# Optimization experiments

Measured on AMD Instinct MI355X. Metric: run time of the kernel, lower is better.

Reference implementation:

```python
import jax, jax.numpy as jnp
import numpy as np

N_NODES = 50000
D = 128
E_RAND = 640000
ALPHA = 0.2  # LeakyReLU negative slope


def setup_inputs() -> dict:
    key = jax.random.key(0)
    k1, k2, k3, k4, k5 = jax.random.split(key, 5)
    inputs = jax.random.normal(k1, (N_NODES, D), dtype=jnp.float32) * 0.1
    # xavier_normal with gain=1.414 as in the torch module
    W = jax.random.normal(k2, (D, D), dtype=jnp.float32) * (1.414 * np.sqrt(2.0 / (D + D)))
    a = jax.random.normal(k3, (2 * D,), dtype=jnp.float32) * (1.414 * np.sqrt(2.0 / (1 + 2 * D)))
    # random edges + self-loops so every node has at least one outgoing edge (nonzero rowsum)
    src = jnp.concatenate([jax.random.randint(k4, (E_RAND,), 0, N_NODES), jnp.arange(N_NODES)])
    dst = jnp.concatenate([jax.random.randint(k5, (E_RAND,), 0, N_NODES), jnp.arange(N_NODES)])
    edge = jnp.stack([src, dst]).astype(jnp.int64)
    return {"inputs": inputs, "edge": edge, "W": W, "a": a}


def reference(inputs, edge, W, a):
    N = inputs.shape[0]
    src, dst = edge[0], edge[1]
    h = inputs @ W  # [N, D]
    # a @ [h_src; h_dst] per edge == h_src @ a[:D] + h_dst @ a[D:]
    score = h[src] @ a[:D] + h[dst] @ a[D:]  # [E]
    edge_e = jnp.exp(jax.nn.leaky_relu(score, negative_slope=ALPHA))  # [E]
    # sparse.mm(coo(edge, edge_e), ones): rowsum over src (coalesce sums duplicates)
    e_rowsum = jax.ops.segment_sum(edge_e, src, num_segments=N)  # [N]
    # sparse.mm(coo(edge, edge_e), h): weighted aggregation of h[dst] into src rows
    h_prime = jax.ops.segment_sum(edge_e[:, None] * h[dst], src, num_segments=N)  # [N, D]
    h_prime = h_prime / e_rowsum[:, None]
    return jax.nn.elu(h_prime)
```

## Files before the change

kernel.cpp:

```cpp
#include <hip/hip_runtime.h>
#include <hip/hip_bf16.h>


constexpr int D    = 128;
constexpr int CH   = 8192;
constexpr int NPB  = 128;
constexpr int CAPB = 2048;

typedef __attribute__((ext_vector_type(8))) short bf16x8;
typedef __attribute__((ext_vector_type(4))) float f32x4;

__device__ __forceinline__ short f2bf(float f) {
    unsigned u = __float_as_uint(f);
    unsigned r = (u + 0x7fffu + ((u >> 16) & 1u)) >> 16;
    return (short)r;
}
__device__ __forceinline__ float bf2f(short b) {
    return __uint_as_float(((unsigned)(unsigned short)b) << 16);
}
__device__ __forceinline__ short2 pk_bf16(float x, float y) {
    __hip_bfloat162 bb = __float22bfloat162_rn(make_float2(x, y));
    short2 r;
    __builtin_memcpy(&r, &bb, 4);
    return r;
}

__global__ __launch_bounds__(256) void init(const float* __restrict__ W,
                                            short* __restrict__ bw,
                                            int* __restrict__ bcnt, int NB) {
    if (blockIdx.x == 8) {
        for (int u = threadIdx.x; u < NB; u += 256) bcnt[u] = 0;
        return;
    }
    const int tid = blockIdx.x * 256 + threadIdx.x;
    const int l = tid & 63, st = tid >> 6;
    const int s = st >> 3, t = st & 7;
    const int n = t * 16 + (l & 15);
    const int q = l >> 4;
#pragma unroll
    for (int j = 0; j < 8; ++j) {
        const int k = s * 32 + q * 8 + j;
        bw[tid * 8 + j] = f2bf(W[k * D + n]);
    }
}

__global__ __launch_bounds__(256) void bin_and_gemm(
    const float* __restrict__ X, const short* __restrict__ bw,
    const float* __restrict__ a,
    const int* __restrict__ src, const int* __restrict__ dst,
    int* __restrict__ bcnt, int* __restrict__ binned,
    short* __restrict__ h, float* __restrict__ s1, float* __restrict__ s2,
    int NB, int NC, int N, int E) {
    __shared__ int hist[392], hbase[392];
    __shared__ short lbw[16384];
    if (blockIdx.x < (unsigned)NC) {
        const int c = blockIdx.x, t = threadIdx.x;
        for (int u = t; u < NB; u += 256) hist[u] = 0;
        __syncthreads();
        const int lo = c * CH, hi = min(lo + CH, E);
        const int hi4 = lo + ((hi - lo) & ~3);
        for (int i = lo + t * 4; i < hi4; i += 1024) {
            const int4 s4 = *(const int4*)(src + i);
            atomicAdd(&hist[s4.x >> 7], 1);
            atomicAdd(&hist[s4.y >> 7], 1);
            atomicAdd(&hist[s4.z >> 7], 1);
            atomicAdd(&hist[s4.w >> 7], 1);
        }
        for (int i = hi4 + t; i < hi; i += 256)
            atomicAdd(&hist[src[i] >> 7], 1);
        __syncthreads();
        for (int u = t; u < NB; u += 256) {
            hbase[u] = atomicAdd(&bcnt[u], hist[u]);
            hist[u] = 0;
        }
        __syncthreads();
        for (int i = lo + t * 4; i < hi4; i += 1024) {
            const int4 s4 = *(const int4*)(src + i);
            const int4 d4 = *(const int4*)(dst + i);
            const int sv[4] = {s4.x, s4.y, s4.z, s4.w};
            const int dv[4] = {d4.x, d4.y, d4.z, d4.w};
#pragma unroll
            for (int j = 0; j < 4; ++j) {
                const int b = sv[j] >> 7;
                const int r = atomicAdd(&hist[b], 1);
                const int idx = hbase[b] + r;
                if (idx < CAPB)
                    binned[b * CAPB + idx] = ((sv[j] & 127) << 16) | dv[j];
            }
        }
        for (int i = hi4 + t; i < hi; i += 256) {
            const int s = src[i];
            const int b = s >> 7;
            const int r = atomicAdd(&hist[b], 1);
            const int idx = hbase[b] + r;
            if (idx < CAPB)
                binned[b * CAPB + idx] = ((s & 127) << 16) | dst[i];
        }
        return;
    }
    {
        int4* lb4 = (int4*)lbw;
        const int4* gb4 = (const int4*)bw;
#pragma unroll
        for (int it = 0; it < 8; ++it)
            lb4[it * 256 + threadIdx.x] = gb4[it * 256 + threadIdx.x];
    }
    __syncthreads();
    const int wave = threadIdx.x >> 6, lane = threadIdx.x & 63;
    const int r0 = (blockIdx.x - NC) * 64 + wave * 16;
    const int m = lane & 15, q = lane >> 4;
    const int arow = r0 + m;
    const bool rowok = arow < N;
    const float* xp = X + (size_t)arow * D + q * 8;

    f32x4 acc[8] = {};
#pragma unroll
    for (int s = 0; s < 4; ++s) {
        float4 xa = {0, 0, 0, 0}, xb = {0, 0, 0, 0};
        if (rowok) {
            xa = *(const float4*)(xp + s * 32);
            xb = *(const float4*)(xp + s * 32 + 4);
        }
        bf16x8 af;
        short2 c0 = pk_bf16(xa.x, xa.y), c1 = pk_bf16(xa.z, xa.w);
        short2 c2 = pk_bf16(xb.x, xb.y), c3 = pk_bf16(xb.z, xb.w);
        af[0] = c0.x; af[1] = c0.y; af[2] = c1.x; af[3] = c1.y;
        af[4] = c2.x; af[5] = c2.y; af[6] = c3.x; af[7] = c3.y;
#pragma unroll
        for (int t = 0; t < 8; ++t) {
            bf16x8 bf = *(const bf16x8*)(lbw + ((s * 8 + t) * 64 + lane) * 8);
            acc[t] = __builtin_amdgcn_mfma_f32_16x16x32_bf16(af, bf, acc[t], 0, 0, 0);
        }
    }
    float a1v[8], a2v[8];
#pragma unroll
    for (int t = 0; t < 8; ++t) {
        a1v[t] = a[t * 16 + m];
        a2v[t] = a[D + t * 16 + m];
    }
    float p1[4] = {0, 0, 0, 0}, p2[4] = {0, 0, 0, 0};
#pragma unroll
    for (int t = 0; t < 8; ++t) {
        short2 h01 = pk_bf16(acc[t][0], acc[t][1]);
        short2 h23 = pk_bf16(acc[t][2], acc[t][3]);
        const short hb[4] = {h01.x, h01.y, h23.x, h23.y};
#pragma unroll
        for (int i = 0; i < 4; ++i) {
            const int row = r0 + q * 4 + i;
            if (row < N) h[(size_t)row * D + t * 16 + m] = hb[i];
            const float hr = bf2f(hb[i]);
            p1[i] += hr * a1v[t];
            p2[i] += hr * a2v[t];
        }
    }
#pragma unroll
    for (int off = 1; off < 16; off <<= 1) {
#pragma unroll
        for (int i = 0; i < 4; ++i) {
            p1[i] += __shfl_xor(p1[i], off);
            p2[i] += __shfl_xor(p2[i], off);
        }
    }
    if (m < 4) {
        const int row = r0 + q * 4 + m;
        if (row < N) {
            const float v1 = (m == 0) ? p1[0] : (m == 1) ? p1[1] : (m == 2) ? p1[2] : p1[3];
            const float v2 = (m == 0) ? p2[0] : (m == 1) ? p2[1] : (m == 2) ? p2[2] : p2[3];
            s1[row] = v1;
            s2[row] = v2;
        }
    }
}

__global__ __launch_bounds__(1024) void aggregate(
    const int* __restrict__ binned, const int* __restrict__ bcnt,
    const float* __restrict__ s1, const float* __restrict__ s2,
    const short* __restrict__ h, float* __restrict__ out, int N) {
    __shared__ int elist[CAPB];
    __shared__ unsigned short dlist[CAPB];
    __shared__ int ncnt[NPB], snc[NPB], exclp[NPB], pcnt[NPB];
    __shared__ float ss1[NPB];
    const int b = blockIdx.x, tid = threadIdx.x;
    const int nb0 = b * NPB;
    if (tid < NPB) {
        ncnt[tid] = 0;
        pcnt[tid] = 0;
        ss1[tid] = (nb0 + tid < N) ? s1[nb0 + tid] : 0.f;
    }
    __syncthreads();
    const int nE = min(bcnt[b], CAPB);
    for (int i = tid; i < nE; i += 1024) {
        const int e = binned[b * CAPB + i];
        elist[i] = e;
        atomicAdd(&ncnt[e >> 16], 1);
    }
    __syncthreads();
    if (tid < NPB) snc[tid] = ncnt[tid];
    __syncthreads();
    for (int o = 1; o < NPB; o <<= 1) {
        const int v = (tid < NPB && tid >= o) ? snc[tid - o] : 0;
        __syncthreads();
        if (tid < NPB) snc[tid] += v;
        __syncthreads();
    }
    if (tid < NPB) exclp[tid] = snc[tid] - ncnt[tid];
    __syncthreads();
    for (int i = tid; i < nE; i += 1024) {
        const int e = elist[i];
        const int r = e >> 16;
        const int k = atomicAdd(&pcnt[r], 1);
        dlist[exclp[r] + k] = (unsigned short)(e & 0xFFFF);
    }
    __syncthreads();

    const int wid = tid >> 6, lane = tid & 63;
    const int g = lane >> 4, m = lane & 15;
#pragma unroll 1
    for (int t = 0; t < 8; ++t) {
        const int r = wid * 8 + t;
        const int n = nb0 + r;
        if (n >= N) continue;
        const int cnt = ncnt[r];
        if (cnt == 0) continue;
        const int beg = exclp[r];
        const float s1n = ss1[r];

        int dA0 = dlist[beg + min(g, cnt - 1)];
        int dB0 = dlist[beg + min(4 + g, cnt - 1)];
        float  sA0 = s2[dA0], sB0 = s2[dB0];
        bf16x8 rA0 = *(const bf16x8*)(h + (size_t)dA0 * D + m * 8);
        bf16x8 rB0 = *(const bf16x8*)(h + (size_t)dB0 * D + m * 8);

        float acc[8] = {};
        float rs = 0.f;
        for (int k0 = 0; k0 < cnt; k0 += 8) {
            const bool more = (k0 + 8) < cnt;
            float sA1, sB1;
            bf16x8 rA1, rB1;
            int dA1, dB1;
            if (more) {
                dA1 = dlist[beg + min(k0 + 8 + g, cnt - 1)];
                dB1 = dlist[beg + min(k0 + 12 + g, cnt - 1)];
                sA1 = s2[dA1];
                sB1 = s2[dB1];
                rA1 = *(const bf16x8*)(h + (size_t)dA1 * D + m * 8);
                rB1 = *(const bf16x8*)(h + (size_t)dB1 * D + m * 8);
            }
            float scA = s1n + sA0;
            scA = scA > 0.f ? scA : 0.2f * scA;
            float eA = __expf(scA);
            if (k0 + g >= cnt) eA = 0.f;
            float scB = s1n + sB0;
            scB = scB > 0.f ? scB : 0.2f * scB;
            float eB = __expf(scB);
            if (k0 + 4 + g >= cnt) eB = 0.f;
#pragma unroll
            for (int j = 0; j < 8; ++j)
                acc[j] += eA * bf2f(rA0[j]) + eB * bf2f(rB0[j]);
            rs += eA + eB;
            if (more) { sA0 = sA1; sB0 = sB1; rA0 = rA1; rB0 = rB1; }
        }
#pragma unroll
        for (int off = 16; off <= 32; off <<= 1) {
            rs += __shfl_xor(rs, off);
#pragma unroll
            for (int j = 0; j < 8; ++j) acc[j] += __shfl_xor(acc[j], off);
        }
        if (g == 0) {
            const float inv = 1.f / rs;
            float o[8];
#pragma unroll
            for (int j = 0; j < 8; ++j) {
                float v = acc[j] * inv;
                o[j] = v > 0.f ? v : expm1f(v);
            }
            float* op = out + (size_t)n * D + m * 8;
            *(float4*)op       = make_float4(o[0], o[1], o[2], o[3]);
            *(float4*)(op + 4) = make_float4(o[4], o[5], o[6], o[7]);
        }
    }
}

extern "C" void kernel_launch(void* const* d_in, const int* in_sizes, int n_in,
                              void* d_out, int out_size, void* d_ws, size_t ws_size,
                              hipStream_t stream) {
    const float* X    = (const float*)d_in[0];
    const int*   edge = (const int*)d_in[1];
    const float* W    = (const float*)d_in[2];
    const float* a    = (const float*)d_in[3];
    float* out = (float*)d_out;

    const int N = in_sizes[0] / D;
    const int E = in_sizes[1] / 2;
    const int* src = edge;
    const int* dst = edge + E;

    const int NB = (N + NPB - 1) / NPB;
    const int NC = (E + CH - 1) / CH;
    const int NG = (N + 63) / 64;

    char* ws = (char*)d_ws;
    short* h    = (short*)ws; ws += (size_t)N * D * sizeof(short);
    int* binned = (int*)ws;   ws += (size_t)NB * CAPB * sizeof(int);
    short* bw   = (short*)ws; ws += 2048 * 8 * sizeof(short);
    float* s1   = (float*)ws; ws += (size_t)N * sizeof(float);
    float* s2   = (float*)ws; ws += (size_t)N * sizeof(float);
    int* bcnt   = (int*)ws;   ws += (size_t)NB * sizeof(int);

    init<<<9, 256, 0, stream>>>(W, bw, bcnt, NB);
    bin_and_gemm<<<NC + NG, 256, 0, stream>>>(X, bw, a, src, dst, bcnt, binned,
                                              h, s1, s2, NB, NC, N, E);
    aggregate<<<NB, 1024, 0, stream>>>(binned, bcnt, s1, s2, h, out, N);
}
```

Before: 145.8 us.

## Split aggregate bins across two 512-thread blocks with wave-shuffle scan

Each 128-node bin is now handled by two 512-thread blocks, each taking 64 nodes and filtering the bin's edges by half. The block-wide LDS prefix scan with many barriers is replaced by a single-wave shuffle scan. The dlist is padded with zeros so the per-edge clamps go away. 32-bit index math and __expf-based ELU replace the size_t math and expm1f. The trade-off is that every edge in a bin is loaded and scanned twice, and ELU loses some precision for small negatives.

Result: faster. 133.9 us (-8.1%).

```diff
diff --git a/kernel.cpp b/kernel.cpp
--- a/kernel.cpp
+++ b/kernel.cpp
@@ -6,6 +6,7 @@
 constexpr int CH   = 8192;
 constexpr int NPB  = 128;
 constexpr int CAPB = 2048;
+constexpr int DCAP = 2064;
 
 typedef __attribute__((ext_vector_type(8))) short bf16x8;
 typedef __attribute__((ext_vector_type(4))) float f32x4;
@@ -172,64 +173,73 @@
     }
 }
 
-__global__ __launch_bounds__(1024) void aggregate(
+__global__ __launch_bounds__(512) void aggregate(
     const int* __restrict__ binned, const int* __restrict__ bcnt,
     const float* __restrict__ s1, const float* __restrict__ s2,
     const short* __restrict__ h, float* __restrict__ out, int N) {
     __shared__ int elist[CAPB];
-    __shared__ unsigned short dlist[CAPB];
-    __shared__ int ncnt[NPB], snc[NPB], exclp[NPB], pcnt[NPB];
-    __shared__ float ss1[NPB];
-    const int b = blockIdx.x, tid = threadIdx.x;
-    const int nb0 = b * NPB;
-    if (tid < NPB) {
+    __shared__ unsigned short dlist[DCAP];
+    __shared__ int ncnt[64], exclp[64], pcnt[64];
+    __shared__ float ss1[64];
+    const int blk = blockIdx.x, tid = threadIdx.x;
+    const int b = blk >> 1, half = blk & 1;
+    const int n0 = b * NPB + half * 64;
+    if (tid < 64) {
         ncnt[tid] = 0;
         pcnt[tid] = 0;
-        ss1[tid] = (nb0 + tid < N) ? s1[nb0 + tid] : 0.f;
+        ss1[tid] = (n0 + tid < N) ? s1[n0 + tid] : 0.f;
     }
     __syncthreads();
     const int nE = min(bcnt[b], CAPB);
-    for (int i = tid; i < nE; i += 1024) {
+    const int hbit = half << 6;
+    for (int i = tid; i < nE; i += 512) {
         const int e = binned[b * CAPB + i];
         elist[i] = e;
-        atomicAdd(&ncnt[e >> 16], 1);
-    }
-    __syncthreads();
-    if (tid < NPB) snc[tid] = ncnt[tid];
-    __syncthreads();
-    for (int o = 1; o < NPB; o <<= 1) {
-        const int v = (tid < NPB && tid >= o) ? snc[tid - o] : 0;
-        __syncthreads();
-        if (tid < NPB) snc[tid] += v;
-        __syncthreads();
-    }
-    if (tid < NPB) exclp[tid] = snc[tid] - ncnt[tid];
-    __syncthreads();
-    for (int i = tid; i < nE; i += 1024) {
+        const int r = e >> 16;
+        if ((r & 64) == hbit) atomicAdd(&ncnt[r & 63], 1);
+    }
+    __syncthreads();
+    if (tid < 64) {
+        int v = ncnt[tid];
+#pragma unroll
+        for (int o = 1; o < 64; o <<= 1) {
+            const int u = __shfl_up(v, o);
+            if (tid >= o) v += u;
+        }
+        exclp[tid] = v - ncnt[tid];
+    }
+    __syncthreads();
+    const int total = exclp[63] + ncnt[63];
+    if (tid < 16) dlist[total + tid] = 0;
+    for (int i = tid; i < nE; i += 512) {
         const int e = elist[i];
         const int r = e >> 16;
-        const int k = atomicAdd(&pcnt[r], 1);
-        dlist[exclp[r] + k] = (unsigned short)(e & 0xFFFF);
+        if ((r & 64) == hbit) {
+            const int rr = r & 63;
+            const int k = atomicAdd(&pcnt[rr], 1);
+            dlist[exclp[rr] + k] = (unsigned short)(e & 0xFFFF);
+        }
     }
     __syncthreads();
 
     const int wid = tid >> 6, lane = tid & 63;
     const int g = lane >> 4, m = lane & 15;
+    const int m8 = m * 8;
 #pragma unroll 1
     for (int t = 0; t < 8; ++t) {
         const int r = wid * 8 + t;
-        const int n = nb0 + r;
+        const int n = n0 + r;
         if (n >= N) continue;
         const int cnt = ncnt[r];
         if (cnt == 0) continue;
         const int beg = exclp[r];
         const float s1n = ss1[r];
 
-        int dA0 = dlist[beg + min(g, cnt - 1)];
-        int dB0 = dlist[beg + min(4 + g, cnt - 1)];
+        int dA0 = dlist[beg + g];
+        int dB0 = dlist[beg + 4 + g];
         float  sA0 = s2[dA0], sB0 = s2[dB0];
-        bf16x8 rA0 = *(const bf16x8*)(h + (size_t)dA0 * D + m * 8);
-        bf16x8 rB0 = *(const bf16x8*)(h + (size_t)dB0 * D + m * 8);
+        bf16x8 rA0 = *(const bf16x8*)(h + (dA0 << 7) + m8);
+        bf16x8 rB0 = *(const bf16x8*)(h + (dB0 << 7) + m8);
 
         float acc[8] = {};
         float rs = 0.f;
@@ -237,14 +247,13 @@
             const bool more = (k0 + 8) < cnt;
             float sA1, sB1;
             bf16x8 rA1, rB1;
-            int dA1, dB1;
             if (more) {
-                dA1 = dlist[beg + min(k0 + 8 + g, cnt - 1)];
-                dB1 = dlist[beg + min(k0 + 12 + g, cnt - 1)];
+                const int dA1 = dlist[beg + k0 + 8 + g];
+                const int dB1 = dlist[beg + k0 + 12 + g];
                 sA1 = s2[dA1];
                 sB1 = s2[dB1];
-                rA1 = *(const bf16x8*)(h + (size_t)dA1 * D + m * 8);
-                rB1 = *(const bf16x8*)(h + (size_t)dB1 * D + m * 8);
+                rA1 = *(const bf16x8*)(h + (dA1 << 7) + m8);
+                rB1 = *(const bf16x8*)(h + (dB1 << 7) + m8);
             }
             float scA = s1n + sA0;
             scA = scA > 0.f ? scA : 0.2f * scA;
@@ -271,10 +280,10 @@
             float o[8];
 #pragma unroll
             for (int j = 0; j < 8; ++j) {
-                float v = acc[j] * inv;
-                o[j] = v > 0.f ? v : expm1f(v);
+                const float v = acc[j] * inv;
+                o[j] = v > 0.f ? v : __expf(v) - 1.f;
             }
-            float* op = out + (size_t)n * D + m * 8;
+            float* op = out + (size_t)n * D + m8;
             *(float4*)op       = make_float4(o[0], o[1], o[2], o[3]);
             *(float4*)(op + 4) = make_float4(o[4], o[5], o[6], o[7]);
         }
@@ -310,5 +319,5 @@
     init<<<9, 256, 0, stream>>>(W, bw, bcnt, NB);
     bin_and_gemm<<<NC + NG, 256, 0, stream>>>(X, bw, a, src, dst, bcnt, binned,
                                               h, s1, s2, NB, NC, N, E);
-    aggregate<<<NB, 1024, 0, stream>>>(binned, bcnt, s1, s2, h, out, N);
-}
+    aggregate<<<NB * 2, 512, 0, stream>>>(binned, bcnt, s1, s2, h, out, N);
+}
```
